# Optimization experiments

Hardware: AMD Instinct MI355X
Metric: run time of the kernel (lower is better)

The kernel has to match this reference:

```python
import jax, jax.numpy as jnp
import numpy as np
from jax import lax

N, CI, CO, H, W = 2, 256, 256, 64, 64
K, G, DIL, PAD, STRIDE = 3, 8, 1, 1, 1
P = K * K
CG = CO // G  # group channels = 32


def setup_inputs() -> dict:
    key = jax.random.key(0)
    ks = jax.random.split(key, 24)
    r = lambda i, shape, s=1.0: jax.random.normal(ks[i], shape, jnp.float32) * s
    u = lambda i, shape: jax.random.uniform(ks[i], shape, jnp.float32, 0.5, 1.5)
    return dict(
        x=r(0, (N, CI, H, W)),
        conv1_w=r(1, (CO, CI), CI ** -0.5),
        bn1_g=u(2, (CO,)), bn1_b=r(3, (CO,), 0.1), bn1_m=r(4, (CO,), 0.1), bn1_v=u(5, (CO,)),
        inproj_w=r(6, (CO, CO), CO ** -0.5), inproj_b=r(7, (CO,), 0.02),
        dw_w=r(8, (CO, 1, K, K), 0.2), dw_b=r(9, (CO,), 0.02),
        ln_g=u(10, (CO,)), ln_b=r(11, (CO,), 0.02),
        off_w=r(12, (CO, G * P * 2), CO ** -0.5), off_b=jnp.zeros((G * P * 2,), jnp.float32),
        mask_w=r(13, (CO, G * P), CO ** -0.5), mask_b=jnp.zeros((G * P,), jnp.float32),
        outproj_w=r(14, (CO, CO), CO ** -0.5), outproj_b=r(15, (CO,), 0.02),
        bn2_g=u(16, (CO,)), bn2_b=r(17, (CO,), 0.1), bn2_m=r(18, (CO,), 0.1), bn2_v=u(19, (CO,)),
    )


def _bn(x, g, b, m, v, eps):
    # inference-mode BatchNorm2d on NCHW
    return (x - m[:, None, None]) * (g[:, None, None] * lax.rsqrt(v[:, None, None] + eps)) + b[:, None, None]


def _dcn_core(t, offset, mask):
    # t: (N,H,W,C) projected input; offset: (N,H,W,G*P*2); mask: (N,H,W,G,P) softmaxed
    xp = jnp.pad(t, ((0, 0), (PAD, PAD), (PAD, PAD), (0, 0)))
    H_, W_ = H + 2 * PAD, W + 2 * PAD
    # reference points (sample centers), normalized to padded size
    ry = ((DIL * (K - 1)) / 2 + 0.5 + STRIDE * jnp.arange(H, dtype=t.dtype)) / H_
    rx = ((DIL * (K - 1)) / 2 + 0.5 + STRIDE * jnp.arange(W, dtype=t.dtype)) / W_
    base = (DIL * (K - 1)) // 2
    gx = jnp.linspace(-base, -base + (K - 1) * DIL, K, dtype=t.dtype) / W_
    gy = jnp.linspace(-base, -base + (K - 1) * DIL, K, dtype=t.dtype) / H_
    gxx, gyy = jnp.meshgrid(gx, gy, indexing='ij')  # x varies along axis 0 (torch meshgrid order)
    grid = jnp.stack([gxx, gyy], -1).reshape(P, 2)  # (P,2)
    off = offset.reshape(N, H, W, G, P, 2) / jnp.array([W_, H_], t.dtype)
    loc_x = rx[None, None, :, None, None] + grid[:, 0][None, None, None, None] + off[..., 0]  # (N,H,W,G,P)
    loc_y = ry[None, :, None, None, None] + grid[:, 1][None, None, None, None] + off[..., 1]
    # grid_sample(align_corners=False): pixel = norm*size - 0.5
    px = jnp.transpose(loc_x * W_ - 0.5, (0, 3, 1, 2, 4)).reshape(N, G, H * W * P)
    py = jnp.transpose(loc_y * H_ - 0.5, (0, 3, 1, 2, 4)).reshape(N, G, H * W * P)
    # grouped channels-last image: (N,G,H_*W_,CG)
    xg = jnp.transpose(xp.reshape(N, H_, W_, G, CG), (0, 3, 1, 2, 4)).reshape(N, G, H_ * W_, CG)
    x0 = jnp.floor(px)
    y0 = jnp.floor(py)
    wx1 = px - x0
    wy1 = py - y0
    x0i = x0.astype(jnp.int32)
    y0i = y0.astype(jnp.int32)

    def corner(xi, yi, w):
        valid = (xi >= 0) & (xi <= W_ - 1) & (yi >= 0) & (yi <= H_ - 1)
        idx = jnp.clip(yi, 0, H_ - 1) * W_ + jnp.clip(xi, 0, W_ - 1)
        v = jnp.take_along_axis(xg, idx[..., None], axis=2)  # (N,G,M,CG)
        return v * jnp.where(valid, w, 0.0)[..., None]

    sampled = (corner(x0i, y0i, (1 - wx1) * (1 - wy1))
               + corner(x0i + 1, y0i, wx1 * (1 - wy1))
               + corner(x0i, y0i + 1, (1 - wx1) * wy1)
               + corner(x0i + 1, y0i + 1, wx1 * wy1))
    sampled = sampled.reshape(N, G, H * W, P, CG)
    mg = jnp.transpose(mask, (0, 3, 1, 2, 4)).reshape(N, G, H * W, P)
    out = jnp.einsum('nglpc,nglp->nglc', sampled, mg)
    return jnp.transpose(out, (0, 2, 1, 3)).reshape(N, H, W, G * CG)


def reference(x, conv1_w, bn1_g, bn1_b, bn1_m, bn1_v, inproj_w, inproj_b, dw_w, dw_b,
              ln_g, ln_b, off_w, off_b, mask_w, mask_b, outproj_w, outproj_b,
              bn2_g, bn2_b, bn2_m, bn2_v):
    # Conv(inc, ouc, k=1): 1x1 conv (no bias) + BN(eps=1e-3) + SiLU
    y = jnp.einsum('nchw,oc->nohw', x, conv1_w)
    y = jax.nn.silu(_bn(y, bn1_g, bn1_b, bn1_m, bn1_v, 1e-3))
    t = jnp.transpose(y, (0, 2, 3, 1))  # NHWC
    xproj = t @ inproj_w + inproj_b     # input_proj Linear
    # offset/mask branch: depthwise conv (k=3,s=1,p=1) -> LN over C -> GELU
    z = lax.conv_general_dilated(y, dw_w, (1, 1), ((PAD, PAD), (PAD, PAD)),
                                 feature_group_count=CO,
                                 dimension_numbers=('NCHW', 'OIHW', 'NCHW')) + dw_b[None, :, None, None]
    z = jnp.transpose(z, (0, 2, 3, 1))
    mu = jnp.mean(z, -1, keepdims=True)
    var = jnp.var(z, -1, keepdims=True)
    z = (z - mu) * lax.rsqrt(var + 1e-5) * ln_g + ln_b
    z = jax.nn.gelu(z, approximate=False)
    offset = z @ off_w + off_b  # (N,H,W,G*P*2)
    mask = jax.nn.softmax((z @ mask_w + mask_b).reshape(N, H, W, G, P), axis=-1)
    s = _dcn_core(xproj, offset, mask)
    s = s @ outproj_w + outproj_b  # output_proj Linear
    o = jnp.transpose(s, (0, 3, 1, 2))  # back to NCHW
    return jax.nn.silu(_bn(o, bn2_g, bn2_b, bn2_m, bn2_v, 1e-5))
```

## Files before the change

kernel.cpp:

```cpp
#include <hip/hip_runtime.h>
#include <hip/hip_fp16.h>
#include <math.h>

#define CC    256
#define HH    64
#define WW    64
#define HWSZ  4096
#define NPIX  8192
#define MT    32
#define TT    16
#define ASTR  264

typedef __attribute__((ext_vector_type(8))) _Float16 half8;
typedef __attribute__((ext_vector_type(4))) float f32x4;

__device__ __forceinline__ float silu_f(float x) { return x / (1.f + __expf(-x)); }

__device__ __forceinline__ short f2h(float f) {
    __half h = __float2half(f);
    return *reinterpret_cast<short*>(&h);
}
__device__ __forceinline__ unsigned h2u(float a, float b) {
    __half2 h = __floats2half2_rn(a, b);
    return *reinterpret_cast<unsigned*>(&h);
}
__device__ __forceinline__ __half2 u2h(unsigned v) { return *reinterpret_cast<__half2*>(&v); }
__device__ __forceinline__ unsigned h2raw(__half2 h) { return *reinterpret_cast<unsigned*>(&h); }
__device__ __forceinline__ float4 h2f4(uint2 u) {
    float2 a = __half22float2(u2h(u.x));
    float2 b = __half22float2(u2h(u.y));
    return make_float4(a.x, a.y, b.x, b.y);
}

__global__ __launch_bounds__(256) void k_prepA(
        const float* __restrict__ cw, const float* __restrict__ ipw,
        const float* __restrict__ dww,
        const float* __restrict__ offb, const float* __restrict__ maskb,
        const float* __restrict__ g1, const float* __restrict__ b1,
        const float* __restrict__ m1, const float* __restrict__ v1,
        const float* __restrict__ g2, const float* __restrict__ b2,
        const float* __restrict__ m2, const float* __restrict__ v2,
        short* __restrict__ Wc1b, short* __restrict__ Wipb,
        float* __restrict__ dwt,
        float* __restrict__ bh, float* __restrict__ sc1, float* __restrict__ sh1,
        float* __restrict__ sc2, float* __restrict__ sh2) {
    __shared__ float tile[64 * 65];
    int t = threadIdx.x, bt = blockIdx.x;
    int ct = t & 63, rb = t >> 6;
    if (bt < 16) {
        int sub = bt;
        int oT = (sub & 3) * 64, cT = (sub >> 2) * 64;
#pragma unroll
        for (int i = 0; i < 16; ++i) {
            int r = rb * 16 + i;
            tile[r * 65 + ct] = ipw[(cT + r) * CC + oT + ct];
        }
        __syncthreads();
#pragma unroll
        for (int i = 0; i < 16; ++i) {
            int r = rb * 16 + i;
            Wipb[(size_t)(oT + r) * CC + cT + ct] = f2h(tile[ct * 65 + r]);
        }
    } else if (bt < 20) {
        int base = (bt - 16) * 16384;
#pragma unroll
        for (int i = 0; i < 16; ++i) {
            int idx = base + i * 1024 + t * 4;
            float4 v = *(const float4*)(cw + idx);
            *(uint2*)(Wc1b + idx) = make_uint2(h2u(v.x, v.y), h2u(v.z, v.w));
        }
    } else {
        int c = t;
#pragma unroll
        for (int j = 0; j < 9; ++j)
            dwt[j * CC + c] = dww[c * 9 + j];
        float bv = 0.f;
        if (c < 144) bv = offb[c];
        else if (c < 216) bv = maskb[c - 144];
        bh[c] = bv;
        float s1 = g1[c] * rsqrtf(v1[c] + 1e-3f);
        sc1[c] = s1; sh1[c] = b1[c] - m1[c] * s1;
        float s2 = g2[c] * rsqrtf(v2[c] + 1e-5f);
        sc2[c] = s2; sh2[c] = b2[c] - m2[c] * s2;
    }
}

__device__ __forceinline__ void gemm1(const short* As, const short* __restrict__ Wb,
                                      int lane, int n0, f32x4* acc) {
    const int m = lane & 15, q = lane >> 4;
#pragma unroll
    for (int kk = 0; kk < 8; ++kk) {
        int c0 = kk * 32 + q * 8;
        half8 a = *(const half8*)(As + m * ASTR + c0);
        half8 b = *(const half8*)(Wb + (size_t)(n0 + m) * CC + c0);
        *acc = __builtin_amdgcn_mfma_f32_16x16x32_f16(a, b, *acc, 0, 0, 0);
    }
}

__global__ __launch_bounds__(1024, 8) void k_conv_in(
        const float* __restrict__ x, const short* __restrict__ Wc1b,
        const short* __restrict__ Wipb, const float* __restrict__ sc1,
        const float* __restrict__ sh1, const float* __restrict__ ipb,
        const float* __restrict__ offw, const float* __restrict__ maskw,
        const float* __restrict__ opw,
        short* __restrict__ Whb, short* __restrict__ Wopb,
        short* __restrict__ ybf, short* __restrict__ xpb) {
    __shared__ __align__(16) short As[MT * ASTR];
    __shared__ float tile[64 * 65];
    int tid = threadIdx.x, lane = tid & 63, wv = tid >> 6;
    int bid = blockIdx.x;

    if (bid >= 256) {
        int t2 = bid - 256;
        int m = t2 >> 4;
        int sub = t2 & 15;
        int oT = (sub & 3) * 64, cT = (sub >> 2) * 64;
        int ct = tid & 63, rb = tid >> 6;
#pragma unroll
        for (int i = 0; i < 4; ++i) {
            int r = rb * 4 + i;
            int c = cT + r, o = oT + ct;
            float v;
            if (m == 1) v = opw[c * CC + o];
            else v = (o < 144) ? offw[c * 144 + o]
                   : (o < 216) ? maskw[c * 72 + (o - 144)] : 0.f;
            tile[r * 65 + ct] = v;
        }
        __syncthreads();
        short* dst = (m == 0) ? Whb : Wopb;
#pragma unroll
        for (int i = 0; i < 4; ++i) {
            int r = rb * 4 + i;
            dst[(size_t)(oT + r) * CC + cT + ct] = f2h(tile[ct * 65 + r]);
        }
        return;
    }

    int pix0 = bid * MT;
    int n = pix0 >> 12, hw0 = pix0 & (HWSZ - 1);
    int n0 = wv * 16;
    const float* xn = x + (size_t)n * CC * HWSZ;
#pragma unroll
    for (int rep = 0; rep < 2; ++rep) {
        int f = tid + rep * 1024;
        int c = f >> 3, i8 = (f & 7) * 4;
        float4 v = *(const float4*)(xn + (size_t)c * HWSZ + hw0 + i8);
        As[(i8 + 0) * ASTR + c] = f2h(v.x);
        As[(i8 + 1) * ASTR + c] = f2h(v.y);
        As[(i8 + 2) * ASTR + c] = f2h(v.z);
        As[(i8 + 3) * ASTR + c] = f2h(v.w);
    }
    __syncthreads();
    f32x4 acc0 = (f32x4){0.f, 0.f, 0.f, 0.f};
    f32x4 acc1 = (f32x4){0.f, 0.f, 0.f, 0.f};
    gemm1(As, Wc1b, lane, n0, &acc0);
    gemm1(As + 16 * ASTR, Wc1b, lane, n0, &acc1);
    __syncthreads();
    int col = lane & 15, qr = (lane >> 4) * 4;
    int o = n0 + col;
    {
        float sc = sc1[o], sh = sh1[o];
#pragma unroll
        for (int r = 0; r < 4; ++r) {
            short v0 = f2h(silu_f(acc0[r] * sc + sh));
            As[(qr + r) * ASTR + o] = v0;
            ybf[(size_t)(pix0 + qr + r) * CC + o] = v0;
            short v1 = f2h(silu_f(acc1[r] * sc + sh));
            As[(16 + qr + r) * ASTR + o] = v1;
            ybf[(size_t)(pix0 + 16 + qr + r) * CC + o] = v1;
        }
    }
    __syncthreads();
    acc0 = (f32x4){0.f, 0.f, 0.f, 0.f};
    acc1 = (f32x4){0.f, 0.f, 0.f, 0.f};
    gemm1(As, Wipb, lane, n0, &acc0);
    gemm1(As + 16 * ASTR, Wipb, lane, n0, &acc1);
    {
        float bo = ipb[o];
#pragma unroll
        for (int r = 0; r < 4; ++r) {
            xpb[(size_t)(pix0 + qr + r) * CC + o] = f2h(acc0[r] + bo);
            xpb[(size_t)(pix0 + 16 + qr + r) * CC + o] = f2h(acc1[r] + bo);
        }
    }
}

__global__ __launch_bounds__(1024, 8) void k_tail(
        const short* __restrict__ ybf, const short* __restrict__ xpb,
        const float* __restrict__ dwt, const float* __restrict__ dwb,
        const float* __restrict__ lng, const float* __restrict__ lnb,
        const short* __restrict__ Whb, const float* __restrict__ bh,
        const short* __restrict__ Wopb, const float* __restrict__ opb,
        const float* __restrict__ sc2, const float* __restrict__ sh2,
        float* __restrict__ out) {
    __shared__ __align__(16) short As[TT * ASTR];
    __shared__ __align__(16) float buf[TT * 260];
    float* ml   = buf;
    float* loff = buf + 1536;
    float* xs   = buf;

    int tid = threadIdx.x, lane = tid & 63, wv = tid >> 6;
    int bid = blockIdx.x;
    int swz = ((bid & 7) << 6) | (bid >> 3);
    int pix0 = swz * TT;
    int n = pix0 >> 12, hw0 = pix0 & (HWSZ - 1);
    int h = hw0 >> 6, w0 = hw0 & 63;
    int c0 = lane * 4;
    int n0 = wv * 16;
    int col = lane & 15, qr = (lane >> 4) * 4;

    {
        float4 dwbv = *(const float4*)(dwb + c0);
        float4 lngv = *(const float4*)(lng + c0);
        float4 lnbv = *(const float4*)(lnb + c0);
        const short* yn = ybf + (size_t)n * HWSZ * CC;
        int pix = wv;
        int w = w0 + pix;
        float4 acc = dwbv;
        bool inter = (h > 0) && (h < HH - 1) && (w0 > 0) && (w0 < WW - TT);
        if (inter) {
#pragma unroll
            for (int ky = 0; ky < 3; ++ky) {
#pragma unroll
                for (int kx = 0; kx < 3; ++kx) {
                    int t = ky * 3 + kx;
                    float4 wt = *(const float4*)(dwt + t * CC + c0);
                    int idx = ((h + ky - 1) << 6) + (w + kx - 1);
                    float4 yv = h2f4(*(const uint2*)(yn + (size_t)idx * CC + c0));
                    acc.x += yv.x * wt.x;
                    acc.y += yv.y * wt.y;
                    acc.z += yv.z * wt.z;
                    acc.w += yv.w * wt.w;
                }
            }
        } else {
#pragma unroll
            for (int ky = 0; ky < 3; ++ky) {
                int yy = h + ky - 1;
                int yc = min(max(yy, 0), HH - 1);
                float vy = (yy == yc) ? 1.f : 0.f;
#pragma unroll
                for (int kx = 0; kx < 3; ++kx) {
                    int xx = w + kx - 1;
                    int xc = min(max(xx, 0), WW - 1);
                    float vm = vy * ((xx == xc) ? 1.f : 0.f);
                    int t = ky * 3 + kx;
                    float4 wt = *(const float4*)(dwt + t * CC + c0);
                    float4 yv = h2f4(*(const uint2*)(yn + (size_t)((yc << 6) + xc) * CC + c0));
                    acc.x += yv.x * wt.x * vm;
                    acc.y += yv.y * wt.y * vm;
                    acc.z += yv.z * wt.z * vm;
                    acc.w += yv.w * wt.w * vm;
                }
            }
        }
        float s1 = acc.x + acc.y + acc.z + acc.w;
        float s2 = acc.x * acc.x + acc.y * acc.y + acc.z * acc.z + acc.w * acc.w;
#pragma unroll
        for (int off = 32; off > 0; off >>= 1) {
            s1 += __shfl_xor(s1, off);
            s2 += __shfl_xor(s2, off);
        }
        float mu = s1 * (1.f / 256.f);
        float var = s2 * (1.f / 256.f) - mu * mu;
        float rs = rsqrtf(var + 1e-5f);
        float4 zv;
        zv.x = (acc.x - mu) * rs * lngv.x + lnbv.x;
        zv.y = (acc.y - mu) * rs * lngv.y + lnbv.y;
        zv.z = (acc.z - mu) * rs * lngv.z + lnbv.z;
        zv.w = (acc.w - mu) * rs * lngv.w + lnbv.w;
        zv.x = 0.5f * zv.x * (1.f + erff(zv.x * 0.70710678118654752f));
        zv.y = 0.5f * zv.y * (1.f + erff(zv.y * 0.70710678118654752f));
        zv.z = 0.5f * zv.z * (1.f + erff(zv.z * 0.70710678118654752f));
        zv.w = 0.5f * zv.w * (1.f + erff(zv.w * 0.70710678118654752f));
        *(uint2*)(As + pix * ASTR + c0) = make_uint2(h2u(zv.x, zv.y), h2u(zv.z, zv.w));
    }
    __syncthreads();

    {
        f32x4 acc = (f32x4){0.f, 0.f, 0.f, 0.f};
        gemm1(As, Whb, lane, n0, &acc);
        int o = n0 + col;
        float bo = bh[o];
#pragma unroll
        for (int r = 0; r < 4; ++r) {
            float v = acc[r] + bo;
            int pix = qr + r;
            if (o < 144) loff[pix * 144 + o] = v;
            else if (o < 216) {
                int mo = o - 144;
                int mg = (mo * 7282) >> 16;
                ml[pix * 96 + mg * 12 + (mo - mg * 9)] = v;
            }
        }
    }
    __syncthreads();

    {
        int g   = lane >> 3;
        int ci  = lane & 7;
        int cq  = ci & 3;
        int par = ci >> 2;
        int gc0 = g * 32 + cq * 8;
        int pix = wv;
        int w = w0 + pix;
        const float* row = ml + pix * 96 + g * 12;
        float4 r0 = *(const float4*)(row);
        float4 r1 = *(const float4*)(row + 4);
        float e0 = __expf(r0.x), e1 = __expf(r0.y), e2 = __expf(r0.z);
        float e3 = __expf(r0.w), e4 = __expf(r1.x), e5 = __expf(r1.y);
        float e6 = __expf(r1.z), e7 = __expf(r1.w), e8 = __expf(row[8]);
        float inv = 1.f / (e0 + e1 + e2 + e3 + e4 + e5 + e6 + e7 + e8);
        float m0 = (par ? e5 : e0) * inv;
        float m1 = (par ? e6 : e1) * inv;
        float m2 = (par ? e7 : e2) * inv;
        float m3 = (par ? e8 : e3) * inv;
        float m4 = e4 * inv;
        const float* lp = loff + pix * 144 + g * 18 + par * 10;
        const short* xpn = xpb + (size_t)n * HWSZ * CC;
        __half2 a0 = u2h(0u), a1 = u2h(0u), a2 = u2h(0u), a3 = u2h(0u);

        auto tapw = [&](float ox, float oy, int tx, int ty, float mval,
                        int& i00, int& i10, int& i01, int& i11,
                        float& w00, float& w10, float& w01, float& w11) {
            float px = (float)(w + tx) + ox;
            float py = (float)(h + ty) + oy;
            float fx = floorf(px), fy = floorf(py);
            float wx1 = px - fx, wy1 = py - fy;
            int x0 = (int)fx, y0 = (int)fy;
            int x1 = x0 + 1, y1 = y0 + 1;
            int xc0 = min(max(x0, 1), WW), xc1 = min(max(x1, 1), WW);
            int yc0 = min(max(y0, 1), HH), yc1 = min(max(y1, 1), HH);
            float vx0 = (x0 == xc0) ? 1.f : 0.f, vx1 = (x1 == xc1) ? 1.f : 0.f;
            float vy0 = (y0 == yc0) ? 1.f : 0.f, vy1 = (y1 == yc1) ? 1.f : 0.f;
            w00 = (1.f - wx1) * (1.f - wy1) * mval * vx0 * vy0;
            w10 = wx1 * (1.f - wy1) * mval * vx1 * vy0;
            w01 = (1.f - wx1) * wy1 * mval * vx0 * vy1;
            w11 = wx1 * wy1 * mval * vx1 * vy1;
            i00 = (((yc0 - 1) << 6) + (xc0 - 1)) * CC + gc0;
            i10 = (((yc0 - 1) << 6) + (xc1 - 1)) * CC + gc0;
            i01 = (((yc1 - 1) << 6) + (xc0 - 1)) * CC + gc0;
            i11 = (((yc1 - 1) << 6) + (xc1 - 1)) * CC + gc0;
        };
        auto fma4 = [&](uint4 u, float wgt) {
            __half2 W = __float2half2_rn(wgt);
            a0 = __hfma2(u2h(u.x), W, a0);
            a1 = __hfma2(u2h(u.y), W, a1);
            a2 = __hfma2(u2h(u.z), W, a2);
            a3 = __hfma2(u2h(u.w), W, a3);
        };

        int A00, A10, A01, A11, B00, B10, B01, B11;
        float Wa0, Wa1, Wa2, Wa3, Wb0, Wb1, Wb2, Wb3;
        float2 ofa = *(const float2*)(lp + 0);
        float2 ofb = *(const float2*)(lp + 2);
        tapw(ofa.x, ofa.y, par ? 1 : 0, par ? 2 : 0, m0, A00, A10, A01, A11, Wa0, Wa1, Wa2, Wa3);
        tapw(ofb.x, ofb.y, par ? 2 : 0, par ? 0 : 1, m1, B00, B10, B01, B11, Wb0, Wb1, Wb2, Wb3);
        {
            uint4 uA0 = *(const uint4*)(xpn + A00);
            uint4 uA1 = *(const uint4*)(xpn + A10);
            uint4 uA2 = *(const uint4*)(xpn + A01);
            uint4 uA3 = *(const uint4*)(xpn + A11);
            uint4 uB0 = *(const uint4*)(xpn + B00);
            uint4 uB1 = *(const uint4*)(xpn + B10);
            uint4 uB2 = *(const uint4*)(xpn + B01);
            uint4 uB3 = *(const uint4*)(xpn + B11);
            fma4(uA0, Wa0); fma4(uA1, Wa1); fma4(uA2, Wa2); fma4(uA3, Wa3);
            fma4(uB0, Wb0); fma4(uB1, Wb1); fma4(uB2, Wb2); fma4(uB3, Wb3);
        }
        ofa = *(const float2*)(lp + 4);
        ofb = *(const float2*)(lp + 6);
        tapw(ofa.x, ofa.y, par ? 2 : 0, par ? 1 : 2, m2, A00, A10, A01, A11, Wa0, Wa1, Wa2, Wa3);
        tapw(ofb.x, ofb.y, par ? 2 : 1, par ? 2 : 0, m3, B00, B10, B01, B11, Wb0, Wb1, Wb2, Wb3);
        {
            uint4 uA0 = *(const uint4*)(xpn + A00);
            uint4 uA1 = *(const uint4*)(xpn + A10);
            uint4 uA2 = *(const uint4*)(xpn + A01);
            uint4 uA3 = *(const uint4*)(xpn + A11);
            uint4 uB0 = *(const uint4*)(xpn + B00);
            uint4 uB1 = *(const uint4*)(xpn + B10);
            uint4 uB2 = *(const uint4*)(xpn + B01);
            uint4 uB3 = *(const uint4*)(xpn + B11);
            fma4(uA0, Wa0); fma4(uA1, Wa1); fma4(uA2, Wa2); fma4(uA3, Wa3);
            fma4(uB0, Wb0); fma4(uB1, Wb1); fma4(uB2, Wb2); fma4(uB3, Wb3);
        }
        if (!par) {
            ofa = *(const float2*)(lp + 8);
            tapw(ofa.x, ofa.y, 1, 1, m4, A00, A10, A01, A11, Wa0, Wa1, Wa2, Wa3);
            uint4 uA0 = *(const uint4*)(xpn + A00);
            uint4 uA1 = *(const uint4*)(xpn + A10);
            uint4 uA2 = *(const uint4*)(xpn + A01);
            uint4 uA3 = *(const uint4*)(xpn + A11);
            fma4(uA0, Wa0); fma4(uA1, Wa1); fma4(uA2, Wa2); fma4(uA3, Wa3);
        }
        a0 = __hadd2(a0, u2h((unsigned)__shfl_xor((int)h2raw(a0), 4)));
        a1 = __hadd2(a1, u2h((unsigned)__shfl_xor((int)h2raw(a1), 4)));
        a2 = __hadd2(a2, u2h((unsigned)__shfl_xor((int)h2raw(a2), 4)));
        a3 = __hadd2(a3, u2h((unsigned)__shfl_xor((int)h2raw(a3), 4)));
        if (!par)
            *(uint4*)(As + pix * ASTR + gc0) =
                make_uint4(h2raw(a0), h2raw(a1), h2raw(a2), h2raw(a3));
    }
    __syncthreads();

    {
        f32x4 acc = (f32x4){0.f, 0.f, 0.f, 0.f};
        gemm1(As, Wopb, lane, n0, &acc);
        int o = n0 + col;
        float bo = opb[o], sc = sc2[o], sh = sh2[o];
#pragma unroll
        for (int r = 0; r < 4; ++r)
            xs[(qr + r) * 260 + o] = silu_f((acc[r] + bo) * sc + sh);
    }
    __syncthreads();

    {
        int i4 = (tid & 3) * 4;
        int o = tid >> 2;
        float* on = out + (size_t)n * CC * HWSZ + hw0 + i4;
        float4 ov;
        ov.x = xs[(i4 + 0) * 260 + o];
        ov.y = xs[(i4 + 1) * 260 + o];
        ov.z = xs[(i4 + 2) * 260 + o];
        ov.w = xs[(i4 + 3) * 260 + o];
        *(float4*)(on + (size_t)o * HWSZ) = ov;
    }
}

extern "C" void kernel_launch(void* const* d_in, const int* in_sizes, int n_in,
                              void* d_out, int out_size, void* d_ws, size_t ws_size,
                              hipStream_t stream) {
    const float* x        = (const float*)d_in[0];
    const float* conv1_w  = (const float*)d_in[1];
    const float* bn1_g    = (const float*)d_in[2];
    const float* bn1_b    = (const float*)d_in[3];
    const float* bn1_m    = (const float*)d_in[4];
    const float* bn1_v    = (const float*)d_in[5];
    const float* inproj_w = (const float*)d_in[6];
    const float* inproj_b = (const float*)d_in[7];
    const float* dw_w     = (const float*)d_in[8];
    const float* dw_b     = (const float*)d_in[9];
    const float* ln_g     = (const float*)d_in[10];
    const float* ln_b     = (const float*)d_in[11];
    const float* off_w    = (const float*)d_in[12];
    const float* off_b    = (const float*)d_in[13];
    const float* mask_w   = (const float*)d_in[14];
    const float* mask_b   = (const float*)d_in[15];
    const float* outproj_w = (const float*)d_in[16];
    const float* outproj_b = (const float*)d_in[17];
    const float* bn2_g    = (const float*)d_in[18];
    const float* bn2_b    = (const float*)d_in[19];
    const float* bn2_m    = (const float*)d_in[20];
    const float* bn2_v    = (const float*)d_in[21];
    float* out = (float*)d_out;

    short* Wc1b = (short*)d_ws;
    short* Wipb = Wc1b + 65536;
    short* Whb  = Wipb + 65536;
    short* Wopb = Whb + 65536;
    float* fp   = (float*)(Wopb + 65536);
    float* dwt  = fp;
    float* bh   = dwt + 9 * CC;
    float* sc1  = bh + 256;
    float* sh1  = sc1 + 256;
    float* sc2  = sh1 + 256;
    float* sh2  = sc2 + 256;
    short* ybf  = (short*)(sh2 + 256);
    short* xpb  = ybf + (size_t)NPIX * CC;

    k_prepA<<<dim3(21), dim3(256), 0, stream>>>(conv1_w, inproj_w, dw_w,
                                                off_b, mask_b, bn1_g, bn1_b, bn1_m, bn1_v,
                                                bn2_g, bn2_b, bn2_m, bn2_v,
                                                Wc1b, Wipb, dwt, bh, sc1, sh1, sc2, sh2);
    k_conv_in<<<dim3(288), dim3(1024), 0, stream>>>(x, Wc1b, Wipb, sc1, sh1, inproj_b,
                                                    off_w, mask_w, outproj_w, Whb, Wopb,
                                                    ybf, xpb);
    k_tail<<<dim3(NPIX / TT), dim3(1024), 0, stream>>>(ybf, xpb, dwt, dw_b, ln_g, ln_b,
                                                       Whb, bh, Wopb, outproj_b, sc2, sh2, out);
}
```

Before: 148.0 us.

## Halve conv_in pixel tile and stage outputs through LDS for coalesced stores

The fused 1x1 conv + input-projection kernel now processes 16 pixels per block instead of 32, doubling the block count from 256 to 512 so more blocks are spread across the CUs. The SiLU output and projection results are first written to shared memory and then stored to global as contiguous 8-byte rows per wave, replacing the old scattered 2-byte strided stores. In exchange, each block loads the weight matrices for half as many pixels, so weight reads from cache double, and extra barriers are added.

```diff
diff --git a/kernel.cpp b/kernel.cpp
--- a/kernel.cpp
+++ b/kernel.cpp
@@ -7,7 +7,7 @@
 #define WW    64
 #define HWSZ  4096
 #define NPIX  8192
-#define MT    32
+#define CT    16
 #define TT    16
 #define ASTR  264
 
@@ -105,13 +105,13 @@
         const float* __restrict__ opw,
         short* __restrict__ Whb, short* __restrict__ Wopb,
         short* __restrict__ ybf, short* __restrict__ xpb) {
-    __shared__ __align__(16) short As[MT * ASTR];
+    __shared__ __align__(16) short As[CT * ASTR];
     __shared__ float tile[64 * 65];
     int tid = threadIdx.x, lane = tid & 63, wv = tid >> 6;
     int bid = blockIdx.x;
 
-    if (bid >= 256) {
-        int t2 = bid - 256;
+    if (bid >= 512) {
+        int t2 = bid - 512;
         int m = t2 >> 4;
         int sub = t2 & 15;
         int oT = (sub & 3) * 64, cT = (sub >> 2) * 64;
@@ -136,53 +136,45 @@
         return;
     }
 
-    int pix0 = bid * MT;
+    int pix0 = bid * CT;
     int n = pix0 >> 12, hw0 = pix0 & (HWSZ - 1);
     int n0 = wv * 16;
     const float* xn = x + (size_t)n * CC * HWSZ;
-#pragma unroll
-    for (int rep = 0; rep < 2; ++rep) {
-        int f = tid + rep * 1024;
-        int c = f >> 3, i8 = (f & 7) * 4;
-        float4 v = *(const float4*)(xn + (size_t)c * HWSZ + hw0 + i8);
-        As[(i8 + 0) * ASTR + c] = f2h(v.x);
-        As[(i8 + 1) * ASTR + c] = f2h(v.y);
-        As[(i8 + 2) * ASTR + c] = f2h(v.z);
-        As[(i8 + 3) * ASTR + c] = f2h(v.w);
-    }
-    __syncthreads();
-    f32x4 acc0 = (f32x4){0.f, 0.f, 0.f, 0.f};
-    f32x4 acc1 = (f32x4){0.f, 0.f, 0.f, 0.f};
-    gemm1(As, Wc1b, lane, n0, &acc0);
-    gemm1(As + 16 * ASTR, Wc1b, lane, n0, &acc1);
+    {
+        int c = tid >> 2, i4 = (tid & 3) * 4;
+        float4 v = *(const float4*)(xn + (size_t)c * HWSZ + hw0 + i4);
+        As[(i4 + 0) * ASTR + c] = f2h(v.x);
+        As[(i4 + 1) * ASTR + c] = f2h(v.y);
+        As[(i4 + 2) * ASTR + c] = f2h(v.z);
+        As[(i4 + 3) * ASTR + c] = f2h(v.w);
+    }
+    __syncthreads();
+    f32x4 acc = (f32x4){0.f, 0.f, 0.f, 0.f};
+    gemm1(As, Wc1b, lane, n0, &acc);
     __syncthreads();
     int col = lane & 15, qr = (lane >> 4) * 4;
     int o = n0 + col;
     {
         float sc = sc1[o], sh = sh1[o];
 #pragma unroll
-        for (int r = 0; r < 4; ++r) {
-            short v0 = f2h(silu_f(acc0[r] * sc + sh));
-            As[(qr + r) * ASTR + o] = v0;
-            ybf[(size_t)(pix0 + qr + r) * CC + o] = v0;
-            short v1 = f2h(silu_f(acc1[r] * sc + sh));
-            As[(16 + qr + r) * ASTR + o] = v1;
-            ybf[(size_t)(pix0 + 16 + qr + r) * CC + o] = v1;
-        }
-    }
-    __syncthreads();
-    acc0 = (f32x4){0.f, 0.f, 0.f, 0.f};
-    acc1 = (f32x4){0.f, 0.f, 0.f, 0.f};
-    gemm1(As, Wipb, lane, n0, &acc0);
-    gemm1(As + 16 * ASTR, Wipb, lane, n0, &acc1);
+        for (int r = 0; r < 4; ++r)
+            As[(qr + r) * ASTR + o] = f2h(silu_f(acc[r] * sc + sh));
+    }
+    __syncthreads();
+    *(uint2*)(ybf + (size_t)(pix0 + wv) * CC + lane * 4) =
+        *(const uint2*)(As + wv * ASTR + lane * 4);
+    acc = (f32x4){0.f, 0.f, 0.f, 0.f};
+    gemm1(As, Wipb, lane, n0, &acc);
+    __syncthreads();
     {
         float bo = ipb[o];
 #pragma unroll
-        for (int r = 0; r < 4; ++r) {
-            xpb[(size_t)(pix0 + qr + r) * CC + o] = f2h(acc0[r] + bo);
-            xpb[(size_t)(pix0 + 16 + qr + r) * CC + o] = f2h(acc1[r] + bo);
-        }
-    }
+        for (int r = 0; r < 4; ++r)
+            As[(qr + r) * ASTR + o] = f2h(acc[r] + bo);
+    }
+    __syncthreads();
+    *(uint2*)(xpb + (size_t)(pix0 + wv) * CC + lane * 4) =
+        *(const uint2*)(As + wv * ASTR + lane * 4);
 }
 
 __global__ __launch_bounds__(1024, 8) void k_tail(
@@ -472,7 +464,7 @@
                                                 off_b, mask_b, bn1_g, bn1_b, bn1_m, bn1_v,
                                                 bn2_g, bn2_b, bn2_m, bn2_v,
                                                 Wc1b, Wipb, dwt, bh, sc1, sh1, sc2, sh2);
-    k_conv_in<<<dim3(288), dim3(1024), 0, stream>>>(x, Wc1b, Wipb, sc1, sh1, inproj_b,
+    k_conv_in<<<dim3(544), dim3(1024), 0, stream>>>(x, Wc1b, Wipb, sc1, sh1, inproj_b,
                                                     off_w, mask_w, outproj_w, Whb, Wopb,
                                                     ybf, xpb);
     k_tail<<<dim3(NPIX / TT), dim3(1024), 0, stream>>>(ybf, xpb, dwt, dw_b, ln_g, ln_b,
```

Result: slower. 158.2 us (+6.9%).
